# Performance work log

Hardware: AMD Instinct MI355X
Metric: run time of the kernel (lower is better)

Reference implementation:

```python
import jax, jax.numpy as jnp
import numpy as np

N = 8192      # nodes
IN = 1433     # input_feat_dim
H1 = 256      # hidden_dim1
H2 = 128      # hidden_dim2
EPS = 1e-5    # BatchNorm1d eps
NEG = -9e15   # GAT mask value
SLOPE = 0.2   # leaky_relu negative slope (gamma)


def setup_inputs() -> dict:
    key = jax.random.key(0)
    ks = jax.random.split(key, 8)
    x = jax.random.normal(ks[0], (N, H2), dtype=jnp.float32)
    u = jax.random.uniform(ks[1], (N, N), dtype=jnp.float32)
    adj = jnp.where(u > 0.999, jnp.float32(0.01), jnp.float32(0.0))
    def w(k, shape):
        fan = shape[0]
        return jax.random.normal(k, shape, dtype=jnp.float32) / jnp.sqrt(jnp.float32(fan))
    return {
        "x": x,
        "adj": adj,
        "W_att": w(ks[2], (H2, H2)),
        "a_att": w(ks[3], (2 * H2, 1)),
        "W_fd1": w(ks[4], (H2, H1)),
        "bn1_g": jnp.ones((H1,), jnp.float32),
        "bn1_b": jnp.zeros((H1,), jnp.float32),
        "W_fd2": w(ks[5], (H1, IN)),
        "bn2_g": jnp.ones((IN,), jnp.float32),
        "bn2_b": jnp.zeros((IN,), jnp.float32),
        "W_sd1": w(ks[6], (H2, H1)),
        "bn3_g": jnp.ones((H1,), jnp.float32),
        "bn3_b": jnp.zeros((H1,), jnp.float32),
    }


def batchnorm(h, g, b):
    # BatchNorm1d training-mode forward: batch stats, biased variance
    m = h.mean(axis=0)
    v = ((h - m) ** 2).mean(axis=0)
    return (h - m) * jax.lax.rsqrt(v + EPS) * g + b


def reference(x, adj, W_att, a_att, W_fd1, bn1_g, bn1_b, W_fd2, bn2_g, bn2_b,
              W_sd1, bn3_g, bn3_b):
    # --- GraphAttentionLayer (concat=False, dropout=0) ---
    Wh = x @ W_att                       # [N, H2]
    f1 = Wh @ a_att[:H2]                 # [N, 1]
    f2 = Wh @ a_att[H2:]                 # [N, 1]
    e = jax.nn.leaky_relu(f1 + f2.T, SLOPE)          # [N, N]
    att = jnp.where(adj > 0, e, jnp.float32(NEG))
    att = jax.nn.softmax(att, axis=1)
    z = att @ Wh                         # condensed encoder output [N, H2]
    # --- feature decoder branch ---
    h1 = jax.nn.relu(adj @ (z @ W_fd1))  # GCN: adj @ (X W), relu
    h1 = batchnorm(h1, bn1_g, bn1_b)
    feat = jax.nn.relu(adj @ (h1 @ W_fd2))
    feat = batchnorm(feat, bn2_g, bn2_b)
    # --- structure decoder branch ---
    s1 = jax.nn.relu(adj @ (z @ W_sd1))
    s1 = batchnorm(s1, bn3_g, bn3_b)
    struct = s1 @ s1.T                   # inner-product decode, identity act [N, N]
    return feat, struct
```

## Files before the change

### kernel.cpp

```cpp
#include <hip/hip_runtime.h>
#include <hip/hip_bf16.h>
#include <stdint.h>

#define NN 8192
#define MAXNZ 64
#define BN_EPS 1e-5f
#define SLOPE 0.2f
#define IND 1433
#define NPAD 1536

typedef float f32x4v __attribute__((ext_vector_type(4)));
typedef short bf16x8v __attribute__((ext_vector_type(8)));

__device__ __forceinline__ float wave_sum(float v) {
#pragma unroll
  for (int off = 32; off > 0; off >>= 1) v += __shfl_xor(v, off);
  return v;
}
__device__ __forceinline__ float wave_max(float v) {
#pragma unroll
  for (int off = 32; off > 0; off >>= 1) v = fmaxf(v, __shfl_xor(v, off));
  return v;
}

#define GLOAD_LDS16(g, l)                                                      \
  __builtin_amdgcn_global_load_lds(                                            \
      (const __attribute__((address_space(1))) unsigned int*)(g),              \
      (__attribute__((address_space(3))) unsigned int*)(l), 16, 0, 0)

__global__ __launch_bounds__(256) void gemm_att_k(const float* __restrict__ A,
                                                  const float* __restrict__ B,
                                                  const float* __restrict__ aatt,
                                                  float* __restrict__ C,
                                                  float* __restrict__ cs,
                                                  float* __restrict__ f1,
                                                  float* __restrict__ f2) {
  __shared__ float As[64][68];
  __shared__ float Bs[64][68];
  __shared__ float csL[64];
  const int t = threadIdx.x;
  const int m0 = blockIdx.x * 64, n0 = blockIdx.y * 64;
  const int tx = t & 15, ty = t >> 4;
  if (t < 64) csL[t] = 0.f;
  float acc[4][4] = {};
  for (int kt = 0; kt < 128; kt += 64) {
    if (kt) __syncthreads();
#pragma unroll
    for (int i = 0; i < 4; ++i) {
      int fid = t + 256 * i;
      int r = fid >> 4, kq = (fid & 15) * 4;
      float4 v = *(const float4*)&A[(size_t)(m0 + r) * 128 + kt + kq];
      *(float4*)&As[r][kq] = v;
    }
#pragma unroll
    for (int i = 0; i < 4; ++i) {
      int fid = t + 256 * i;
      int r = fid >> 4, cq = (fid & 15) * 4;
      float4 v = *(const float4*)&B[(size_t)(kt + r) * 128 + n0 + cq];
      *(float4*)&Bs[r][cq] = v;
    }
    __syncthreads();
#pragma unroll 4
    for (int k0 = 0; k0 < 64; k0 += 4) {
      float4 a[4], b[4];
#pragma unroll
      for (int i = 0; i < 4; ++i) a[i] = *(const float4*)&As[ty * 4 + i][k0];
#pragma unroll
      for (int j = 0; j < 4; ++j) b[j] = *(const float4*)&Bs[k0 + j][tx * 4];
#pragma unroll
      for (int kk = 0; kk < 4; ++kk) {
#pragma unroll
        for (int i = 0; i < 4; ++i) {
          float av = ((const float*)&a[i])[kk];
#pragma unroll
          for (int j = 0; j < 4; ++j)
            acc[i][j] += av * ((const float*)&b[kk])[j];
        }
      }
    }
  }
#pragma unroll
  for (int i = 0; i < 4; ++i) {
    float4 v = make_float4(acc[i][0], acc[i][1], acc[i][2], acc[i][3]);
    *(float4*)&C[(size_t)(m0 + ty * 4 + i) * 128 + n0 + tx * 4] = v;
  }
  float a1v[4], a2v[4];
#pragma unroll
  for (int j = 0; j < 4; ++j) {
    a1v[j] = aatt[n0 + tx * 4 + j];
    a2v[j] = aatt[128 + n0 + tx * 4 + j];
  }
#pragma unroll
  for (int i = 0; i < 4; ++i) {
    float p1 = acc[i][0] * a1v[0] + acc[i][1] * a1v[1] + acc[i][2] * a1v[2] +
               acc[i][3] * a1v[3];
    float p2 = acc[i][0] * a2v[0] + acc[i][1] * a2v[1] + acc[i][2] * a2v[2] +
               acc[i][3] * a2v[3];
#pragma unroll
    for (int off = 1; off < 16; off <<= 1) {
      p1 += __shfl_xor(p1, off);
      p2 += __shfl_xor(p2, off);
    }
    if ((t & 15) == 0) {
      atomicAdd(&f1[m0 + ty * 4 + i], p1);
      atomicAdd(&f2[m0 + ty * 4 + i], p2);
    }
  }
  float cp[4];
#pragma unroll
  for (int j = 0; j < 4; ++j) {
    cp[j] = acc[0][j] + acc[1][j] + acc[2][j] + acc[3][j];
    cp[j] += __shfl_xor(cp[j], 16);
    cp[j] += __shfl_xor(cp[j], 32);
  }
  if ((t & 63) < 16) {
#pragma unroll
    for (int j = 0; j < 4; ++j) atomicAdd(&csL[(t & 15) * 4 + j], cp[j]);
  }
  __syncthreads();
  if (t < 64) atomicAdd(&cs[n0 + t], csL[t]);
}

__global__ void extract_attn_k(const float* __restrict__ adj, const float* __restrict__ Wh,
                               const float* __restrict__ f1, const float* __restrict__ f2,
                               const float* __restrict__ cs, int* __restrict__ nnzA,
                               int* __restrict__ idxA, float* __restrict__ valA,
                               float* __restrict__ valsumA, float* __restrict__ z) {
  __shared__ int idxL[4][MAXNZ];
  __shared__ float valL[4][MAXNZ];
  int l = threadIdx.x & 63, w = threadIdx.x >> 6;
  int i = blockIdx.x * 4 + w;
  const float* row = adj + (size_t)i * NN;
  int base = 0;
  for (int it = 0; it < NN / 256; ++it) {
    float4 v4 = *(const float4*)&row[it * 256 + l * 4];
#pragma unroll
    for (int j = 0; j < 4; ++j) {
      float v = ((const float*)&v4)[j];
      bool p = v > 0.0f;
      unsigned long long m = __ballot(p);
      if (p) {
        int pos = base + (int)__popcll(m & ((1ull << l) - 1ull));
        if (pos < MAXNZ) {
          idxL[w][pos] = it * 256 + l * 4 + j;
          valL[w][pos] = v;
        }
      }
      base += (int)__popcll(m);
    }
  }
  int nnz = base < MAXNZ ? base : MAXNZ;
  if (l == 0) nnzA[i] = nnz;
  __syncthreads();

  int c = -1;
  float v = 0.f, att = 0.f;
  if (l < nnz) { c = idxL[w][l]; v = valL[w][l]; }
  idxA[(size_t)i * MAXNZ + l] = (l < nnz) ? c : 0;
  valA[(size_t)i * MAXNZ + l] = v;
  float vs = wave_sum(v);
  if (l == 0) valsumA[i] = vs;

  if (nnz == 0) {
    const float inv = 1.0f / 8192.0f;
    z[(size_t)i * 128 + l] = cs[l] * inv;
    z[(size_t)i * 128 + 64 + l] = cs[64 + l] * inv;
    return;
  }
  float e = -INFINITY;
  if (l < nnz) {
    float u = f1[i] + f2[c];
    e = u >= 0.f ? u : SLOPE * u;
  }
  float mx = wave_max(e);
  float p = (l < nnz) ? expf(e - mx) : 0.f;
  float s = wave_sum(p);
  att = p / s;
  float a0 = 0.f, a1 = 0.f;
  for (int j = 0; j < nnz; ++j) {
    float wt = __shfl(att, j);
    int r = __shfl(c, j);
    a0 += wt * Wh[(size_t)r * 128 + l];
    a1 += wt * Wh[(size_t)r * 128 + 64 + l];
  }
  z[(size_t)i * 128 + l] = a0;
  z[(size_t)i * 128 + 64 + l] = a1;
}

__global__ void gather_z_k(const float* __restrict__ X, const int* __restrict__ nnzA,
                           const int* __restrict__ idxA, const float* __restrict__ valA,
                           __hip_bfloat16* __restrict__ Y) {
  int l = threadIdx.x & 63, w = threadIdx.x >> 6;
  int i = blockIdx.x * 4 + w;
  int nnz = nnzA[i];
  float a0 = 0.f, a1 = 0.f;
  for (int j = 0; j < nnz; ++j) {
    int r = idxA[(size_t)i * MAXNZ + j];
    float v = valA[(size_t)i * MAXNZ + j];
    a0 += v * X[(size_t)r * 128 + l];
    a1 += v * X[(size_t)r * 128 + 64 + l];
  }
  Y[(size_t)i * 128 + l] = __float2bfloat16(a0);
  Y[(size_t)i * 128 + 64 + l] = __float2bfloat16(a1);
}

__global__ void s1_gather_k(const __hip_bfloat16* __restrict__ t, const int* __restrict__ nnzA,
                            const int* __restrict__ idxA, const float* __restrict__ valA,
                            const float* __restrict__ valsumA, const float* __restrict__ sums,
                            const float* __restrict__ sumsq, const float* __restrict__ g1,
                            const float* __restrict__ b1, const float* __restrict__ g3,
                            const float* __restrict__ b3, __hip_bfloat16* __restrict__ s1b,
                            __hip_bfloat16* __restrict__ ghb) {
  __shared__ int idxL[MAXNZ];
  __shared__ float valL[MAXNZ];
  int i = blockIdx.x, tt = threadIdx.x;
  int nnz = nnzA[i];
  if (tt < MAXNZ) {
    idxL[tt] = idxA[(size_t)i * MAXNZ + tt];
    valL[tt] = valA[(size_t)i * MAXNZ + tt];
  }
  __syncthreads();
  {
    float m = sums[256 + tt] * (1.f / 8192.f);
    float va = fmaxf(sumsq[256 + tt] * (1.f / 8192.f) - m * m, 0.f);
    float sc = g3[tt] * rsqrtf(va + BN_EPS);
    float sh = b3[tt] - m * sc;
    float v = __bfloat162float(t[(size_t)i * 512 + 256 + tt]) * sc + sh;
    s1b[(size_t)i * 256 + tt] = __float2bfloat16(v);
  }
  float acc = 0.f;
  for (int j = 0; j < nnz; ++j)
    acc += valL[j] * __bfloat162float(t[(size_t)idxL[j] * 512 + tt]);
  float m = sums[tt] * (1.f / 8192.f);
  float va = fmaxf(sumsq[tt] * (1.f / 8192.f) - m * m, 0.f);
  float sc = g1[tt] * rsqrtf(va + BN_EPS);
  float sh = b1[tt] - m * sc;
  ghb[(size_t)i * 256 + tt] = __float2bfloat16(acc * sc + sh * valsumA[i]);
}

__global__ void feat_apply_k(const __hip_bfloat16* __restrict__ fp, const float* __restrict__ sums,
                             const float* __restrict__ sumsq, const float* __restrict__ g,
                             const float* __restrict__ b, float* __restrict__ out) {
  int i = blockIdx.x;
  for (int c = threadIdx.x; c < IND; c += 256) {
    float m = sums[c] * (1.f / 8192.f);
    float va = fmaxf(sumsq[c] * (1.f / 8192.f) - m * m, 0.f);
    float sc = g[c] * rsqrtf(va + BN_EPS);
    float sh = b[c] - m * sc;
    out[(size_t)i * IND + c] = __bfloat162float(fp[(size_t)i * NPAD + c]) * sc + sh;
  }
}

__global__ void prep_k(const float* __restrict__ W_fd2, const float* __restrict__ W_fd1,
                       const float* __restrict__ W_sd1, __hip_bfloat16* __restrict__ Wt,
                       __hip_bfloat16* __restrict__ Wcatb) {
  int b = blockIdx.x, t = threadIdx.x;
  int o = b * 256 + t;
  int n = o >> 8, k = o & 255;
  Wt[o] = __float2bfloat16(n < IND ? W_fd2[(size_t)k * IND + n] : 0.f);
  if (b < 256) {
    int nn = o >> 7, kk = o & 127;
    float v = nn < 256 ? W_fd1[(size_t)kk * 256 + nn] : W_sd1[(size_t)kk * 256 + (nn - 256)];
    Wcatb[o] = __float2bfloat16(v);
  }
}

template <int KT>
__global__ __launch_bounds__(256) void mfma_bt_k(const short* __restrict__ A,
                                                 const short* __restrict__ Bt,
                                                 __hip_bfloat16* __restrict__ C, int ldc,
                                                 int gridN, float* __restrict__ sums,
                                                 float* __restrict__ sumsq) {
  __shared__ short lds[2][16384];
  const int nwg = gridDim.x;
  const int cpx = nwg >> 3;
  const int bid = blockIdx.x;
  const int wg = (bid & 7) * cpx + (bid >> 3);
  const int m0 = (wg / gridN) * 128, n0 = (wg % gridN) * 128;
  const int t = threadIdx.x;
  const int l = t & 63, w = t >> 6;
  const int wm = w >> 1, wn = w & 1;
  const int KW = KT * 128;
  f32x4v acc[4][4];
#pragma unroll
  for (int i = 0; i < 4; ++i)
#pragma unroll
    for (int j = 0; j < 4; ++j)
#pragma unroll
      for (int q = 0; q < 4; ++q) acc[i][j][q] = 0.f;

  for (int kt = 0; kt < KT; ++kt) {
    if (kt) __syncthreads();
#pragma unroll
    for (int i = 0; i < 8; ++i) {
      int region = w * 8 + i;
      int lr = region * 4 + (l >> 4);
      int ch = (l & 15) ^ (lr & 7);
      const short* gA = A + ((size_t)(m0 + lr) * KW + kt * 128 + ch * 8);
      GLOAD_LDS16(gA, &lds[0][region * 512]);
      const short* gB = Bt + ((size_t)(n0 + lr) * KW + kt * 128 + ch * 8);
      GLOAD_LDS16(gB, &lds[1][region * 512]);
    }
    __syncthreads();
#pragma unroll
    for (int ks = 0; ks < 4; ++ks) {
      bf16x8v af[4], bf[4];
#pragma unroll
      for (int mi = 0; mi < 4; ++mi) {
        int lr = wm * 64 + mi * 16 + (l & 15);
        int ch = (ks * 4 + (l >> 4)) ^ (lr & 7);
        af[mi] = *(const bf16x8v*)&lds[0][lr * 128 + ch * 8];
      }
#pragma unroll
      for (int nj = 0; nj < 4; ++nj) {
        int lr = wn * 64 + nj * 16 + (l & 15);
        int ch = (ks * 4 + (l >> 4)) ^ (lr & 7);
        bf[nj] = *(const bf16x8v*)&lds[1][lr * 128 + ch * 8];
      }
#pragma unroll
      for (int mi = 0; mi < 4; ++mi)
#pragma unroll
        for (int nj = 0; nj < 4; ++nj)
          acc[mi][nj] = __builtin_amdgcn_mfma_f32_16x16x32_bf16(
              af[mi], bf[nj], acc[mi][nj], 0, 0, 0);
    }
  }
#pragma unroll
  for (int nj = 0; nj < 4; ++nj) {
    int col = n0 + wn * 64 + nj * 16 + (l & 15);
    float s = 0.f, ss = 0.f;
#pragma unroll
    for (int mi = 0; mi < 4; ++mi) {
#pragma unroll
      for (int q = 0; q < 4; ++q) {
        int row = m0 + wm * 64 + mi * 16 + (l >> 4) * 4 + q;
        float v = fmaxf(acc[mi][nj][q], 0.f);
        C[(size_t)row * ldc + col] = __float2bfloat16(v);
        s += v;
        ss += v * v;
      }
    }
    s += __shfl_xor(s, 16);
    s += __shfl_xor(s, 32);
    ss += __shfl_xor(ss, 16);
    ss += __shfl_xor(ss, 32);
    if ((l >> 4) == 0) {
      atomicAdd(&sums[col], s);
      atomicAdd(&sumsq[col], ss);
    }
  }
}

__global__ __launch_bounds__(256) void tail_k(const short* __restrict__ Agh,
                                              const short* __restrict__ Wt,
                                              __hip_bfloat16* __restrict__ featb,
                                              float* __restrict__ sums,
                                              float* __restrict__ sumsq,
                                              const short* __restrict__ S,
                                              float* __restrict__ C) {
  __shared__ short lds[2][16384];
  const int bid = blockIdx.x;
  const int fA = bid * 24 / 89;
  const int fB = (bid + 1) * 24 / 89;
  const bool isFeat = fB > fA;
  const int t = threadIdx.x;
  const int l = t & 63, w = t >> 6;
  const int wm = w >> 1, wn = w & 1;
  f32x4v acc[4][4];
#pragma unroll
  for (int i = 0; i < 4; ++i)
#pragma unroll
    for (int j = 0; j < 4; ++j)
#pragma unroll
      for (int q = 0; q < 4; ++q) acc[i][j][q] = 0.f;

  if (isFeat) {
    const int fb = fA;
    const int wg = (fb & 7) * 96 + (fb >> 3);
    const int m0 = (wg / 12) * 128, n0 = (wg % 12) * 128;
    for (int kt = 0; kt < 2; ++kt) {
      if (kt) __syncthreads();
#pragma unroll
      for (int i = 0; i < 8; ++i) {
        int region = w * 8 + i;
        int lr = region * 4 + (l >> 4);
        int ch = (l & 15) ^ (lr & 7);
        const short* gA = Agh + ((size_t)(m0 + lr) * 256 + kt * 128 + ch * 8);
        GLOAD_LDS16(gA, &lds[0][region * 512]);
        const short* gB = Wt + ((size_t)(n0 + lr) * 256 + kt * 128 + ch * 8);
        GLOAD_LDS16(gB, &lds[1][region * 512]);
      }
      __syncthreads();
#pragma unroll
      for (int ks = 0; ks < 4; ++ks) {
        bf16x8v af[4], bf[4];
#pragma unroll
        for (int mi = 0; mi < 4; ++mi) {
          int lr = wm * 64 + mi * 16 + (l & 15);
          int ch = (ks * 4 + (l >> 4)) ^ (lr & 7);
          af[mi] = *(const bf16x8v*)&lds[0][lr * 128 + ch * 8];
        }
#pragma unroll
        for (int nj = 0; nj < 4; ++nj) {
          int lr = wn * 64 + nj * 16 + (l & 15);
          int ch = (ks * 4 + (l >> 4)) ^ (lr & 7);
          bf[nj] = *(const bf16x8v*)&lds[1][lr * 128 + ch * 8];
        }
#pragma unroll
        for (int mi = 0; mi < 4; ++mi)
#pragma unroll
          for (int nj = 0; nj < 4; ++nj)
            acc[mi][nj] = __builtin_amdgcn_mfma_f32_16x16x32_bf16(
                af[mi], bf[nj], acc[mi][nj], 0, 0, 0);
      }
    }
#pragma unroll
    for (int nj = 0; nj < 4; ++nj) {
      int col = n0 + wn * 64 + nj * 16 + (l & 15);
      float s = 0.f, ss = 0.f;
#pragma unroll
      for (int mi = 0; mi < 4; ++mi) {
#pragma unroll
        for (int q = 0; q < 4; ++q) {
          int row = m0 + wm * 64 + mi * 16 + (l >> 4) * 4 + q;
          float v = fmaxf(acc[mi][nj][q], 0.f);
          featb[(size_t)row * NPAD + col] = __float2bfloat16(v);
          s += v;
          ss += v * v;
        }
      }
      s += __shfl_xor(s, 16);
      s += __shfl_xor(s, 32);
      ss += __shfl_xor(ss, 16);
      ss += __shfl_xor(ss, 32);
      if ((l >> 4) == 0) {
        atomicAdd(&sums[col], s);
        atomicAdd(&sumsq[col], ss);
      }
    }
  } else {
    const int sb = bid - fA;
    const int wg = (sb & 7) * 260 + (sb >> 3);
    int bi = (int)((129.0f - sqrtf(16641.0f - 8.0f * (float)wg)) * 0.5f);
    while ((bi + 1) * 64 - ((bi + 1) * bi) / 2 <= wg) ++bi;
    while (bi * 64 - (bi * (bi - 1)) / 2 > wg) --bi;
    const int bj = bi + (wg - (bi * 64 - (bi * (bi - 1)) / 2));
    const int m0 = bi * 128, n0 = bj * 128;
    for (int kt = 0; kt < 2; ++kt) {
      if (kt) __syncthreads();
#pragma unroll
      for (int i = 0; i < 8; ++i) {
        int region = w * 8 + i;
        int lr = region * 4 + (l >> 4);
        int ch = (l & 15) ^ (lr & 7);
        const short* gA = S + ((size_t)(m0 + lr) * 256 + kt * 128 + ch * 8);
        GLOAD_LDS16(gA, &lds[0][region * 512]);
        const short* gB = S + ((size_t)(n0 + lr) * 256 + kt * 128 + ch * 8);
        GLOAD_LDS16(gB, &lds[1][region * 512]);
      }
      __syncthreads();
#pragma unroll
      for (int ks = 0; ks < 4; ++ks) {
        bf16x8v af[4], bf[4];
#pragma unroll
        for (int mi = 0; mi < 4; ++mi) {
          int lr = wm * 64 + mi * 16 + (l & 15);
          int ch = (ks * 4 + (l >> 4)) ^ (lr & 7);
          af[mi] = *(const bf16x8v*)&lds[0][lr * 128 + ch * 8];
        }
#pragma unroll
        for (int nj = 0; nj < 4; ++nj) {
          int lr = wn * 64 + nj * 16 + (l & 15);
          int ch = (ks * 4 + (l >> 4)) ^ (lr & 7);
          bf[nj] = *(const bf16x8v*)&lds[1][lr * 128 + ch * 8];
        }
#pragma unroll
        for (int mi = 0; mi < 4; ++mi)
#pragma unroll
          for (int nj = 0; nj < 4; ++nj)
            acc[mi][nj] = __builtin_amdgcn_mfma_f32_16x16x32_bf16(
                af[mi], bf[nj], acc[mi][nj], 0, 0, 0);
      }
    }
#pragma unroll
    for (int mi = 0; mi < 4; ++mi) {
#pragma unroll
      for (int nj = 0; nj < 4; ++nj) {
        int col = n0 + wn * 64 + nj * 16 + (l & 15);
#pragma unroll
        for (int q = 0; q < 4; ++q) {
          int row = m0 + wm * 64 + mi * 16 + (l >> 4) * 4 + q;
          C[(size_t)row * NN + col] = acc[mi][nj][q];
        }
      }
    }
    if (bi != bj) {
#pragma unroll
      for (int nj = 0; nj < 4; ++nj) {
        int col = n0 + wn * 64 + nj * 16 + (l & 15);
#pragma unroll
        for (int mi = 0; mi < 4; ++mi) {
          int row0 = m0 + wm * 64 + mi * 16 + (l >> 4) * 4;
          float4 v = make_float4(acc[mi][nj][0], acc[mi][nj][1], acc[mi][nj][2],
                                 acc[mi][nj][3]);
          *(float4*)&C[(size_t)col * NN + row0] = v;
        }
      }
    }
  }
}

extern "C" void kernel_launch(void* const* d_in, const int* in_sizes, int n_in,
                              void* d_out, int out_size, void* d_ws, size_t ws_size,
                              hipStream_t stream) {
  const float* x = (const float*)d_in[0];
  const float* adj = (const float*)d_in[1];
  const float* W_att = (const float*)d_in[2];
  const float* a_att = (const float*)d_in[3];
  const float* W_fd1 = (const float*)d_in[4];
  const float* bn1g = (const float*)d_in[5];
  const float* bn1b = (const float*)d_in[6];
  const float* W_fd2 = (const float*)d_in[7];
  const float* bn2g = (const float*)d_in[8];
  const float* bn2b = (const float*)d_in[9];
  const float* W_sd1 = (const float*)d_in[10];
  const float* bn3g = (const float*)d_in[11];
  const float* bn3b = (const float*)d_in[12];

  float* out = (float*)d_out;
  float* feat_out = out;
  float* struct_out = out + (size_t)NN * IND;

  float* ws = (float*)d_ws;
  size_t off = 0;
  auto alloc = [&](size_t nfloats) {
    float* p = ws + off;
    off += (nfloats + 255) & ~(size_t)255;
    return p;
  };
  float* Wh = alloc((size_t)NN * 128);
  float* z = alloc((size_t)NN * 128);
  float* valsum = alloc(NN);
  const size_t ZTOT = 256 + 8192 + 8192 + 512 + 512 + 1536 + 1536;
  float* zbase = alloc(ZTOT);
  float* cs = zbase;
  float* f1 = zbase + 256;
  float* f2 = zbase + 256 + 8192;
  float* sumsA = zbase + 256 + 16384;
  float* sumsqA = sumsA + 512;
  float* sumsB = sumsqA + 512;
  float* sumsqB = sumsB + 1536;
  float* valA = alloc((size_t)NN * MAXNZ);
  int* idxA = (int*)alloc((size_t)NN * MAXNZ);
  int* nnzA = (int*)alloc(NN);
  __hip_bfloat16* tbuf = (__hip_bfloat16*)alloc((size_t)NN * 256);
  __hip_bfloat16* gb = (__hip_bfloat16*)alloc((size_t)NN * 64);
  __hip_bfloat16* s1b = (__hip_bfloat16*)alloc((size_t)NN * 128);
  __hip_bfloat16* ghb = (__hip_bfloat16*)alloc((size_t)NN * 128);
  __hip_bfloat16* Wt = (__hip_bfloat16*)alloc((size_t)NPAD * 128);
  __hip_bfloat16* Wcatb = (__hip_bfloat16*)alloc(512 * 64);
  __hip_bfloat16* featb = (__hip_bfloat16*)alloc((size_t)NN * NPAD / 2);

  hipMemsetAsync(zbase, 0, ZTOT * sizeof(float), stream);

  prep_k<<<NPAD, 256, 0, stream>>>(W_fd2, W_fd1, W_sd1, Wt, Wcatb);

  gemm_att_k<<<dim3(NN / 64, 2), 256, 0, stream>>>(x, W_att, a_att, Wh, cs, f1, f2);
  extract_attn_k<<<NN / 4, 256, 0, stream>>>(adj, Wh, f1, f2, cs, nnzA, idxA, valA,
                                             valsum, z);
  gather_z_k<<<NN / 4, 256, 0, stream>>>(z, nnzA, idxA, valA, gb);

  mfma_bt_k<1><<<64 * 4, 256, 0, stream>>>((const short*)gb, (const short*)Wcatb,
                                           tbuf, 512, 4, sumsA, sumsqA);
  s1_gather_k<<<NN, 256, 0, stream>>>(tbuf, nnzA, idxA, valA, valsum, sumsA, sumsqA,
                                      bn1g, bn1b, bn3g, bn3b, s1b, ghb);

  tail_k<<<2848, 256, 0, stream>>>((const short*)ghb, (const short*)Wt, featb,
                                   sumsB, sumsqB, (const short*)s1b, struct_out);
  feat_apply_k<<<NN, 256, 0, stream>>>(featb, sumsB, sumsqB, bn2g, bn2b, feat_out);
}
```

Before: 247.7 us.

## Merge weight prep into attention GEMM, speed adjacency scan, shuffle gather indices

Fuses the weight transpose/convert kernel into the attention GEMM launch as extra blocks, removing one launch. The adjacency row scan now reads 8 floats per lane and skips ballot work when all of them are zero, compacting nonzeros through an LDS atomic counter. Because of that counter, neighbour order is no longer deterministic, so the float summation order can change between runs. The gather kernel loads each row's index and value list once per lane and broadcasts entries with shuffles instead of reloading them every iteration. The __syncthreads after compaction is removed, which looks safe only because each wave uses its own LDS slice.

```diff
diff --git a/kernel.cpp b/kernel.cpp
--- a/kernel.cpp
+++ b/kernel.cpp
@@ -28,18 +28,32 @@
       (const __attribute__((address_space(1))) unsigned int*)(g),              \
       (__attribute__((address_space(3))) unsigned int*)(l), 16, 0, 0)
 
-__global__ __launch_bounds__(256) void gemm_att_k(const float* __restrict__ A,
-                                                  const float* __restrict__ B,
-                                                  const float* __restrict__ aatt,
-                                                  float* __restrict__ C,
-                                                  float* __restrict__ cs,
-                                                  float* __restrict__ f1,
-                                                  float* __restrict__ f2) {
+__global__ __launch_bounds__(256) void prep_gemm_k(
+    const float* __restrict__ A, const float* __restrict__ B,
+    const float* __restrict__ aatt, const float* __restrict__ W_fd2,
+    const float* __restrict__ W_fd1, const float* __restrict__ W_sd1,
+    __hip_bfloat16* __restrict__ Wt, __hip_bfloat16* __restrict__ Wcatb,
+    float* __restrict__ C, float* __restrict__ cs, float* __restrict__ f1,
+    float* __restrict__ f2) {
   __shared__ float As[64][68];
   __shared__ float Bs[64][68];
   __shared__ float csL[64];
+  const int b = blockIdx.x;
   const int t = threadIdx.x;
-  const int m0 = blockIdx.x * 64, n0 = blockIdx.y * 64;
+  if (b < NPAD) {
+    int o = b * 256 + t;
+    int n = o >> 8, k = o & 255;
+    Wt[o] = __float2bfloat16(n < IND ? W_fd2[(size_t)k * IND + n] : 0.f);
+    if (b < 256) {
+      int nn = o >> 7, kk = o & 127;
+      float v = nn < 256 ? W_fd1[(size_t)kk * 256 + nn]
+                         : W_sd1[(size_t)kk * 256 + (nn - 256)];
+      Wcatb[o] = __float2bfloat16(v);
+    }
+    return;
+  }
+  const int bx = b - NPAD;
+  const int m0 = (bx & 127) * 64, n0 = (bx >> 7) * 64;
   const int tx = t & 15, ty = t >> 4;
   if (t < 64) csL[t] = 0.f;
   float acc[4][4] = {};
@@ -62,11 +76,11 @@
     __syncthreads();
 #pragma unroll 4
     for (int k0 = 0; k0 < 64; k0 += 4) {
-      float4 a[4], b[4];
+      float4 a[4], bb[4];
 #pragma unroll
       for (int i = 0; i < 4; ++i) a[i] = *(const float4*)&As[ty * 4 + i][k0];
 #pragma unroll
-      for (int j = 0; j < 4; ++j) b[j] = *(const float4*)&Bs[k0 + j][tx * 4];
+      for (int j = 0; j < 4; ++j) bb[j] = *(const float4*)&Bs[k0 + j][tx * 4];
 #pragma unroll
       for (int kk = 0; kk < 4; ++kk) {
 #pragma unroll
@@ -74,7 +88,7 @@
           float av = ((const float*)&a[i])[kk];
 #pragma unroll
           for (int j = 0; j < 4; ++j)
-            acc[i][j] += av * ((const float*)&b[kk])[j];
+            acc[i][j] += av * ((const float*)&bb[kk])[j];
         }
       }
     }
@@ -126,32 +140,41 @@
                                const float* __restrict__ cs, int* __restrict__ nnzA,
                                int* __restrict__ idxA, float* __restrict__ valA,
                                float* __restrict__ valsumA, float* __restrict__ z) {
+  __shared__ int cntL[4];
   __shared__ int idxL[4][MAXNZ];
   __shared__ float valL[4][MAXNZ];
   int l = threadIdx.x & 63, w = threadIdx.x >> 6;
   int i = blockIdx.x * 4 + w;
+  if (l == 0) cntL[w] = 0;
   const float* row = adj + (size_t)i * NN;
-  int base = 0;
-  for (int it = 0; it < NN / 256; ++it) {
-    float4 v4 = *(const float4*)&row[it * 256 + l * 4];
-#pragma unroll
-    for (int j = 0; j < 4; ++j) {
-      float v = ((const float*)&v4)[j];
-      bool p = v > 0.0f;
-      unsigned long long m = __ballot(p);
-      if (p) {
-        int pos = base + (int)__popcll(m & ((1ull << l) - 1ull));
-        if (pos < MAXNZ) {
-          idxL[w][pos] = it * 256 + l * 4 + j;
-          valL[w][pos] = v;
-        }
-      }
-      base += (int)__popcll(m);
-    }
-  }
-  int nnz = base < MAXNZ ? base : MAXNZ;
+  for (int it = 0; it < NN / 512; ++it) {
+    int c0 = it * 512 + l * 8;
+    float4 va = *(const float4*)&row[c0];
+    float4 vb = *(const float4*)&row[c0 + 4];
+    float mx = fmaxf(fmaxf(fmaxf(va.x, va.y), fmaxf(va.z, va.w)),
+                     fmaxf(fmaxf(vb.x, vb.y), fmaxf(vb.z, vb.w)));
+    if (mx > 0.f) {
+#pragma unroll
+      for (int j = 0; j < 4; ++j) {
+        float v = ((const float*)&va)[j];
+        if (v > 0.f) {
+          int s = atomicAdd(&cntL[w], 1);
+          if (s < MAXNZ) { idxL[w][s] = c0 + j; valL[w][s] = v; }
+        }
+      }
+#pragma unroll
+      for (int j = 0; j < 4; ++j) {
+        float v = ((const float*)&vb)[j];
+        if (v > 0.f) {
+          int s = atomicAdd(&cntL[w], 1);
+          if (s < MAXNZ) { idxL[w][s] = c0 + 4 + j; valL[w][s] = v; }
+        }
+      }
+    }
+  }
+  int nnz = cntL[w];
+  nnz = nnz < MAXNZ ? nnz : MAXNZ;
   if (l == 0) nnzA[i] = nnz;
-  __syncthreads();
 
   int c = -1;
   float v = 0.f, att = 0.f;
@@ -193,10 +216,12 @@
   int l = threadIdx.x & 63, w = threadIdx.x >> 6;
   int i = blockIdx.x * 4 + w;
   int nnz = nnzA[i];
+  int myi = idxA[(size_t)i * MAXNZ + l];
+  float myv = valA[(size_t)i * MAXNZ + l];
   float a0 = 0.f, a1 = 0.f;
   for (int j = 0; j < nnz; ++j) {
-    int r = idxA[(size_t)i * MAXNZ + j];
-    float v = valA[(size_t)i * MAXNZ + j];
+    int r = __shfl(myi, j);
+    float v = __shfl(myv, j);
     a0 += v * X[(size_t)r * 128 + l];
     a1 += v * X[(size_t)r * 128 + 64 + l];
   }
@@ -248,20 +273,6 @@
     float sc = g[c] * rsqrtf(va + BN_EPS);
     float sh = b[c] - m * sc;
     out[(size_t)i * IND + c] = __bfloat162float(fp[(size_t)i * NPAD + c]) * sc + sh;
-  }
-}
-
-__global__ void prep_k(const float* __restrict__ W_fd2, const float* __restrict__ W_fd1,
-                       const float* __restrict__ W_sd1, __hip_bfloat16* __restrict__ Wt,
-                       __hip_bfloat16* __restrict__ Wcatb) {
-  int b = blockIdx.x, t = threadIdx.x;
-  int o = b * 256 + t;
-  int n = o >> 8, k = o & 255;
-  Wt[o] = __float2bfloat16(n < IND ? W_fd2[(size_t)k * IND + n] : 0.f);
-  if (b < 256) {
-    int nn = o >> 7, kk = o & 127;
-    float v = nn < 256 ? W_fd1[(size_t)kk * 256 + nn] : W_sd1[(size_t)kk * 256 + (nn - 256)];
-    Wcatb[o] = __float2bfloat16(v);
   }
 }
 
@@ -563,9 +574,9 @@
 
   hipMemsetAsync(zbase, 0, ZTOT * sizeof(float), stream);
 
-  prep_k<<<NPAD, 256, 0, stream>>>(W_fd2, W_fd1, W_sd1, Wt, Wcatb);
-
-  gemm_att_k<<<dim3(NN / 64, 2), 256, 0, stream>>>(x, W_att, a_att, Wh, cs, f1, f2);
+  prep_gemm_k<<<NPAD + 256, 256, 0, stream>>>(x, W_att, a_att, W_fd2, W_fd1, W_sd1,
+                                              Wt, Wcatb, Wh, cs, f1, f2);
+
   extract_attn_k<<<NN / 4, 256, 0, stream>>>(adj, Wh, f1, f2, cs, nnzA, idxA, valA,
                                              valsum, z);
   gather_z_k<<<NN / 4, 256, 0, stream>>>(z, nnzA, idxA, valA, gb);
```

New measurement: 249.7 us. Within noise of the previous version (+0.8%).

## Load tail GEMM fragments directly from global memory, drop LDS staging

Applied to the files above, without the earlier changes.

The tail kernel (feature decoder GEMM plus symmetric s1·s1ᵀ tiles) stops staging A/B tiles through LDS with barriers. Each wave now reads its bf16 MFMA fragments straight from global/L2, and launch_bounds is raised to ask for 4 blocks per CU. This removes the syncthreads and LDS traffic and lets more blocks run at once, at the cost of redundant global loads across waves and uncoalesced 16-byte row reads. Separately, gather_z_k loads each row's index/value list once per lane and broadcasts it with shuffles instead of re-reading global memory every iteration.

```diff
diff --git a/kernel.cpp b/kernel.cpp
--- a/kernel.cpp
+++ b/kernel.cpp
@@ -193,10 +193,12 @@
   int l = threadIdx.x & 63, w = threadIdx.x >> 6;
   int i = blockIdx.x * 4 + w;
   int nnz = nnzA[i];
+  int myi = idxA[(size_t)i * MAXNZ + l];
+  float myv = valA[(size_t)i * MAXNZ + l];
   float a0 = 0.f, a1 = 0.f;
   for (int j = 0; j < nnz; ++j) {
-    int r = idxA[(size_t)i * MAXNZ + j];
-    float v = valA[(size_t)i * MAXNZ + j];
+    int r = __shfl(myi, j);
+    float v = __shfl(myv, j);
     a0 += v * X[(size_t)r * 128 + l];
     a1 += v * X[(size_t)r * 128 + 64 + l];
   }
@@ -351,69 +353,74 @@
   }
 }
 
-__global__ __launch_bounds__(256) void tail_k(const short* __restrict__ Agh,
-                                              const short* __restrict__ Wt,
-                                              __hip_bfloat16* __restrict__ featb,
-                                              float* __restrict__ sums,
-                                              float* __restrict__ sumsq,
-                                              const short* __restrict__ S,
-                                              float* __restrict__ C) {
-  __shared__ short lds[2][16384];
+__global__ __launch_bounds__(256, 4) void tail_k(const short* __restrict__ Agh,
+                                                 const short* __restrict__ Wt,
+                                                 __hip_bfloat16* __restrict__ featb,
+                                                 float* __restrict__ sums,
+                                                 float* __restrict__ sumsq,
+                                                 const short* __restrict__ S,
+                                                 float* __restrict__ C) {
   const int bid = blockIdx.x;
   const int fA = bid * 24 / 89;
-  const int fB = (bid + 1) * 24 / 89;
-  const bool isFeat = fB > fA;
+  const bool isFeat = ((bid + 1) * 24 / 89) > fA;
   const int t = threadIdx.x;
   const int l = t & 63, w = t >> 6;
   const int wm = w >> 1, wn = w & 1;
-  f32x4v acc[4][4];
-#pragma unroll
-  for (int i = 0; i < 4; ++i)
-#pragma unroll
-    for (int j = 0; j < 4; ++j)
-#pragma unroll
-      for (int q = 0; q < 4; ++q) acc[i][j][q] = 0.f;
-
+
+  const short* Ab;
+  const short* Bb;
+  int m0, n0, bi = 0, bj = 0;
   if (isFeat) {
     const int fb = fA;
     const int wg = (fb & 7) * 96 + (fb >> 3);
-    const int m0 = (wg / 12) * 128, n0 = (wg % 12) * 128;
-    for (int kt = 0; kt < 2; ++kt) {
-      if (kt) __syncthreads();
-#pragma unroll
-      for (int i = 0; i < 8; ++i) {
-        int region = w * 8 + i;
-        int lr = region * 4 + (l >> 4);
-        int ch = (l & 15) ^ (lr & 7);
-        const short* gA = Agh + ((size_t)(m0 + lr) * 256 + kt * 128 + ch * 8);
-        GLOAD_LDS16(gA, &lds[0][region * 512]);
-        const short* gB = Wt + ((size_t)(n0 + lr) * 256 + kt * 128 + ch * 8);
-        GLOAD_LDS16(gB, &lds[1][region * 512]);
-      }
-      __syncthreads();
-#pragma unroll
-      for (int ks = 0; ks < 4; ++ks) {
-        bf16x8v af[4], bf[4];
-#pragma unroll
-        for (int mi = 0; mi < 4; ++mi) {
-          int lr = wm * 64 + mi * 16 + (l & 15);
-          int ch = (ks * 4 + (l >> 4)) ^ (lr & 7);
-          af[mi] = *(const bf16x8v*)&lds[0][lr * 128 + ch * 8];
-        }
-#pragma unroll
-        for (int nj = 0; nj < 4; ++nj) {
-          int lr = wn * 64 + nj * 16 + (l & 15);
-          int ch = (ks * 4 + (l >> 4)) ^ (lr & 7);
-          bf[nj] = *(const bf16x8v*)&lds[1][lr * 128 + ch * 8];
-        }
-#pragma unroll
-        for (int mi = 0; mi < 4; ++mi)
-#pragma unroll
-          for (int nj = 0; nj < 4; ++nj)
-            acc[mi][nj] = __builtin_amdgcn_mfma_f32_16x16x32_bf16(
-                af[mi], bf[nj], acc[mi][nj], 0, 0, 0);
-      }
-    }
+    m0 = (wg / 12) * 128;
+    n0 = (wg % 12) * 128;
+    Ab = Agh;
+    Bb = Wt;
+  } else {
+    const int sb = bid - fA;
+    const int wg = (sb & 7) * 260 + (sb >> 3);
+    bi = (int)((129.0f - sqrtf(16641.0f - 8.0f * (float)wg)) * 0.5f);
+    while ((bi + 1) * 64 - ((bi + 1) * bi) / 2 <= wg) ++bi;
+    while (bi * 64 - (bi * (bi - 1)) / 2 > wg) --bi;
+    bj = bi + (wg - (bi * 64 - (bi * (bi - 1)) / 2));
+    m0 = bi * 128;
+    n0 = bj * 128;
+    Ab = S;
+    Bb = S;
+  }
+
+  f32x4v acc[4][4];
+#pragma unroll
+  for (int i = 0; i < 4; ++i)
+#pragma unroll
+    for (int j = 0; j < 4; ++j)
+#pragma unroll
+      for (int q = 0; q < 4; ++q) acc[i][j][q] = 0.f;
+
+#pragma unroll
+  for (int ks = 0; ks < 8; ++ks) {
+    const int kcol = ks * 32 + (l >> 4) * 8;
+    bf16x8v af[4], bf[4];
+#pragma unroll
+    for (int mi = 0; mi < 4; ++mi) {
+      int row = m0 + wm * 64 + mi * 16 + (l & 15);
+      af[mi] = *(const bf16x8v*)&Ab[(size_t)row * 256 + kcol];
+    }
+#pragma unroll
+    for (int nj = 0; nj < 4; ++nj) {
+      int row = n0 + wn * 64 + nj * 16 + (l & 15);
+      bf[nj] = *(const bf16x8v*)&Bb[(size_t)row * 256 + kcol];
+    }
+#pragma unroll
+    for (int mi = 0; mi < 4; ++mi)
+#pragma unroll
+      for (int nj = 0; nj < 4; ++nj)
+        acc[mi][nj] = __builtin_amdgcn_mfma_f32_16x16x32_bf16(
+            af[mi], bf[nj], acc[mi][nj], 0, 0, 0);
+  }
+
+  if (isFeat) {
 #pragma unroll
     for (int nj = 0; nj < 4; ++nj) {
       int col = n0 + wn * 64 + nj * 16 + (l & 15);
@@ -439,49 +446,6 @@
       }
     }
   } else {
-    const int sb = bid - fA;
-    const int wg = (sb & 7) * 260 + (sb >> 3);
-    int bi = (int)((129.0f - sqrtf(16641.0f - 8.0f * (float)wg)) * 0.5f);
-    while ((bi + 1) * 64 - ((bi + 1) * bi) / 2 <= wg) ++bi;
-    while (bi * 64 - (bi * (bi - 1)) / 2 > wg) --bi;
-    const int bj = bi + (wg - (bi * 64 - (bi * (bi - 1)) / 2));
-    const int m0 = bi * 128, n0 = bj * 128;
-    for (int kt = 0; kt < 2; ++kt) {
-      if (kt) __syncthreads();
-#pragma unroll
-      for (int i = 0; i < 8; ++i) {
-        int region = w * 8 + i;
-        int lr = region * 4 + (l >> 4);
-        int ch = (l & 15) ^ (lr & 7);
-        const short* gA = S + ((size_t)(m0 + lr) * 256 + kt * 128 + ch * 8);
-        GLOAD_LDS16(gA, &lds[0][region * 512]);
-        const short* gB = S + ((size_t)(n0 + lr) * 256 + kt * 128 + ch * 8);
-        GLOAD_LDS16(gB, &lds[1][region * 512]);
-      }
-      __syncthreads();
-#pragma unroll
-      for (int ks = 0; ks < 4; ++ks) {
-        bf16x8v af[4], bf[4];
-#pragma unroll
-        for (int mi = 0; mi < 4; ++mi) {
-          int lr = wm * 64 + mi * 16 + (l & 15);
-          int ch = (ks * 4 + (l >> 4)) ^ (lr & 7);
-          af[mi] = *(const bf16x8v*)&lds[0][lr * 128 + ch * 8];
-        }
-#pragma unroll
-        for (int nj = 0; nj < 4; ++nj) {
-          int lr = wn * 64 + nj * 16 + (l & 15);
-          int ch = (ks * 4 + (l >> 4)) ^ (lr & 7);
-          bf[nj] = *(const bf16x8v*)&lds[1][lr * 128 + ch * 8];
-        }
-#pragma unroll
-        for (int mi = 0; mi < 4; ++mi)
-#pragma unroll
-          for (int nj = 0; nj < 4; ++nj)
-            acc[mi][nj] = __builtin_amdgcn_mfma_f32_16x16x32_bf16(
-                af[mi], bf[nj], acc[mi][nj], 0, 0, 0);
-      }
-    }
 #pragma unroll
     for (int mi = 0; mi < 4; ++mi) {
 #pragma unroll
```

New measurement: 297.9 us. 20.2% more time.
